# Kernel optimization log

Measured on AMD Instinct MI355X. Metric: run time of the kernel, lower is better.

Reference implementation:

```python
import jax, jax.numpy as jnp
import numpy as np

B, T, D_MODEL, HEAD_DIM = 4, 4096, 1024, 64

def setup_inputs() -> dict:
    key = jax.random.key(0)
    ks = jax.random.split(key, 7)
    s = 1.0 / np.sqrt(D_MODEL)
    return {
        "x": jax.random.normal(ks[0], (B, T, D_MODEL), dtype=jnp.float32),
        "Wq": jax.random.uniform(ks[1], (D_MODEL, HEAD_DIM), jnp.float32, -s, s),
        "bq": jax.random.uniform(ks[2], (HEAD_DIM,), jnp.float32, -s, s),
        "Wk": jax.random.uniform(ks[3], (D_MODEL, HEAD_DIM), jnp.float32, -s, s),
        "bk": jax.random.uniform(ks[4], (HEAD_DIM,), jnp.float32, -s, s),
        "Wv": jax.random.uniform(ks[5], (D_MODEL, HEAD_DIM), jnp.float32, -s, s),
        "bv": jax.random.uniform(ks[6], (HEAD_DIM,), jnp.float32, -s, s),
    }

def reference(x, Wq, bq, Wk, bk, Wv, bv):
    # x: [B,T,D]; projections -> [B,T,H]
    q = jnp.einsum("btd,dh->bth", x, Wq) + bq
    k = jnp.einsum("btd,dh->bth", x, Wk) + bk
    v = jnp.einsum("btd,dh->bth", x, Wv) + bv
    scale = HEAD_DIM ** -0.5
    # scores: [B,Tq,Tk] -- naive full attention matrix (memory-bound)
    scores = jnp.einsum("bqh,bkh->bqk", q, k) * scale
    neg = jnp.finfo(scores.dtype).min
    T_ = scores.shape[-1]
    causal = jnp.triu(jnp.full((T_, T_), neg, dtype=scores.dtype), k=1)
    scores = scores + causal[None, :, :]
    probs = jax.nn.softmax(scores, axis=-1)
    y = jnp.einsum("bqk,bkh->bqh", probs, v)
    return y
```

## Files before the change

### kernel.cpp

```cpp
#include <hip/hip_runtime.h>
#include <hip/hip_bf16.h>

typedef __attribute__((ext_vector_type(4))) float f4v;
typedef __attribute__((ext_vector_type(16))) float f16v;
typedef __attribute__((ext_vector_type(4))) unsigned short u16x4;
typedef __attribute__((ext_vector_type(8))) unsigned short u16x8;
typedef __attribute__((ext_vector_type(4))) unsigned int u32x4;
typedef __attribute__((ext_vector_type(8))) __bf16 bf16x8;
typedef __attribute__((ext_vector_type(8))) _Float16 h8v;

#define D_MODEL 1024
#define HDIM 64
#define TSEQ 4096
#define QB 32
#define KVB 64
#define QSCALE 0.18033688011112042f

__device__ __forceinline__ unsigned short f2bf(float f) {
    union { float f; unsigned u; } v; v.f = f;
    unsigned r = v.u + 0x7FFFu + ((v.u >> 16) & 1u);
    return (unsigned short)(r >> 16);
}
__device__ __forceinline__ bf16x8 ld8(const unsigned short* p) {
    return __builtin_bit_cast(bf16x8, *(const u16x8*)p);
}
__device__ __forceinline__ h8v ldh8(const unsigned short* p) {
    return __builtin_bit_cast(h8v, *(const u16x8*)p);
}
__device__ __forceinline__ f4v mfma16f(h8v a, h8v b, f4v c) {
    return __builtin_amdgcn_mfma_f32_16x16x32_f16(a, b, c, 0, 0, 0);
}
__device__ __forceinline__ f16v mfma32(bf16x8 a, bf16x8 b, f16v c) {
    return __builtin_amdgcn_mfma_f32_32x32x16_bf16(a, b, c, 0, 0, 0);
}
__device__ __forceinline__ unsigned cvtpk(float a, float b) {
    unsigned r;
    asm("v_cvt_pk_bf16_f32 %0, %1, %2" : "=v"(r) : "v"(a), "v"(b));
    return r;
}
__device__ __forceinline__ void pswap(unsigned& a, unsigned& b) {
    asm("v_permlane32_swap_b32 %0, %1" : "+v"(a), "+v"(b));
}
__device__ __forceinline__ h8v pack8(f4v a, f4v b) {
    unsigned p0 = __builtin_bit_cast(unsigned, __builtin_amdgcn_cvt_pkrtz(a[0], a[1]));
    unsigned p1 = __builtin_bit_cast(unsigned, __builtin_amdgcn_cvt_pkrtz(a[2], a[3]));
    unsigned p2 = __builtin_bit_cast(unsigned, __builtin_amdgcn_cvt_pkrtz(b[0], b[1]));
    unsigned p3 = __builtin_bit_cast(unsigned, __builtin_amdgcn_cvt_pkrtz(b[2], b[3]));
    u32x4 u = {p0, p1, p2, p3};
    return __builtin_bit_cast(h8v, u);
}

__global__ void prep_wf(const float* __restrict__ Wq, const float* __restrict__ Wk,
                        const float* __restrict__ Wv, unsigned short* __restrict__ Wf)
{
    int idx = blockIdx.x * 256 + threadIdx.x;
    int j = idx & 7, lane = (idx >> 3) & 63, nf = (idx >> 9) & 3,
        kstep = (idx >> 11) & 31, m = idx >> 16;
    int k = kstep * 32 + 8 * (lane >> 4) + j;
    int n = nf * 16 + (lane & 15);
    const float* W = (m == 0) ? Wq : (m == 1) ? Wk : Wv;
    _Float16 hv = (_Float16)W[k * 64 + n];
    Wf[idx] = __builtin_bit_cast(unsigned short, hv);
}

__global__ __launch_bounds__(256, 2)
void proj_qkv(const float* __restrict__ x, const unsigned short* __restrict__ Wf,
              const float* __restrict__ bq, const float* __restrict__ bk,
              const float* __restrict__ bv,
              unsigned short* __restrict__ Qf, unsigned short* __restrict__ Kf,
              unsigned short* __restrict__ Vf)
{
    __shared__ float xs[2][2048];
    __shared__ unsigned short wl[2][12288];

    const int tid = threadIdx.x;
    const int w = tid >> 6, l = tid & 63;
    const int row0 = blockIdx.x * 32;

    f4v acc[2][3];
#pragma unroll
    for (int s = 0; s < 2; ++s)
#pragma unroll
        for (int f = 0; f < 3; ++f) acc[s][f] = (f4v)0.f;

    auto stage = [&](int buf, int t) {
#pragma unroll
        for (int j = 0; j < 2; ++j) {
            const int G = j * 256 + tid;
            const int row = G >> 4;
            const int gl = (G & 15) ^ (row & 7);
            const float* src = x + (size_t)(row0 + row) * D_MODEL + t * 64 + gl * 4;
            __builtin_amdgcn_global_load_lds(
                (const __attribute__((address_space(1))) unsigned*)src,
                (__attribute__((address_space(3))) unsigned*)&xs[buf][G * 4],
                16, 0, 0);
        }
#pragma unroll
        for (int j = 0; j < 6; ++j) {
            const int chunk = j * 4 + w;
            const int cf = chunk >> 1, ks = chunk & 1;
            const unsigned short* src =
                Wf + ((((cf >> 2) * 32 + (t * 2 + ks)) * 4 + (cf & 3)) << 9) + l * 8;
            __builtin_amdgcn_global_load_lds(
                (const __attribute__((address_space(1))) unsigned*)src,
                (__attribute__((address_space(3))) unsigned*)&wl[buf][chunk * 512],
                16, 0, 0);
        }
    };

    stage(0, 0);
    __syncthreads();

#pragma unroll
    for (int t = 0; t < 16; ++t) {
        if (t < 15) stage((t + 1) & 1, t + 1);
        const int b = t & 1;
        const int sw = l & 7;
#pragma unroll
        for (int ks = 0; ks < 2; ++ks) {
            h8v bw[3];
#pragma unroll
            for (int f = 0; f < 3; ++f) {
                const int cf = w * 3 + f;
                bw[f] = ldh8(&wl[b][(cf * 2 + ks) * 512 + l * 8]);
            }
            const int gr = ks * 8 + 2 * (l >> 4);
#pragma unroll
            for (int s = 0; s < 2; ++s) {
                const int row = s * 16 + (l & 15);
                f4v a0 = *(const f4v*)&xs[b][row * 64 + ((gr ^ sw) << 2)];
                f4v a1 = *(const f4v*)&xs[b][row * 64 + (((gr + 1) ^ sw) << 2)];
                h8v xa = pack8(a0, a1);
#pragma unroll
                for (int f = 0; f < 3; ++f)
                    acc[s][f] = mfma16f(xa, bw[f], acc[s][f]);
            }
        }
        __syncthreads();
    }

    const float* bias[3] = {bq, bk, bv};
#pragma unroll
    for (int s = 0; s < 2; ++s) {
        const int rowb = row0 + s * 16 + 4 * (l >> 4);
        const int b = rowb >> 12, tok0 = rowb & 4095;
#pragma unroll
        for (int f = 0; f < 3; ++f) {
            const int cf = w * 3 + f;
            const int m = cf >> 2, nf = cf & 3;
            const int d = nf * 16 + (l & 15);
            const float bb = bias[m][d];
            if (m == 0) {
                const int qtile = tok0 >> 5;
                const int ksq = d >> 4, hq = (d >> 3) & 1, jq = d & 7;
#pragma unroll
                for (int r4 = 0; r4 < 4; ++r4) {
                    int cq = (tok0 & 31) + r4;
                    Qf[(((size_t)(b * 128 + qtile) * 4 + ksq) << 9) + (32 * hq + cq) * 8 + jq] =
                        f2bf((acc[s][f][r4] + bb) * QSCALE);
                }
            } else if (m == 1) {
                const int t = tok0 >> 6, tb = (tok0 >> 5) & 1;
                const int ksk = d >> 4, hk = (d >> 3) & 1, jk = d & 7;
#pragma unroll
                for (int r4 = 0; r4 < 4; ++r4) {
                    int ck = (tok0 & 31) + r4;
                    Kf[(((size_t)((b * 64 + t) * 8 + tb * 4 + ksk)) << 9) + (32 * hk + ck) * 8 + jk] =
                        f2bf(acc[s][f][r4] + bb);
                }
            } else {
                const int t = tok0 >> 6, ku = (tok0 >> 4) & 3, hv = (tok0 >> 3) & 1, jv = tok0 & 7;
                const int cv = d & 31, td = d >> 5;
                u16x4 pk;
#pragma unroll
                for (int r4 = 0; r4 < 4; ++r4) pk[r4] = f2bf(acc[s][f][r4] + bb);
                *(u16x4*)(Vf + (((size_t)((b * 64 + t) * 8 + td * 4 + ku)) << 9) +
                          (32 * hv + cv) * 8 + jv) = pk;
            }
        }
    }
}

struct TState { float m, l; f16v o0, o1; };

__device__ __forceinline__ void run_tile(const unsigned short* __restrict__ Qf,
                                         const unsigned short* __restrict__ Kf,
                                         const unsigned short* __restrict__ Vf,
                                         int batch, int qt, int g8, int l, int h, int c,
                                         TState& st)
{
    const int NT = (qt >> 1) + 1;
    st.m = -1e30f; st.l = 0.f; st.o0 = (f16v)0.f; st.o1 = (f16v)0.f;

    bf16x8 qf[4];
    const unsigned short* qp = Qf + (((size_t)(batch * 128 + qt) * 4) << 9) + l * 8;
#pragma unroll
    for (int ks = 0; ks < 4; ++ks) qf[ks] = ld8(qp + (ks << 9));

    if (g8 >= NT) return;

    auto kload = [&](bf16x8(&kr)[2][4], int t_) {
        const unsigned short* p = Kf + (((size_t)(batch * 64 + t_) * 8) << 9) + l * 8;
#pragma unroll
        for (int tb = 0; tb < 2; ++tb)
#pragma unroll
            for (int ks = 0; ks < 4; ++ks)
                kr[tb][ks] = ld8(p + ((tb * 4 + ks) << 9));
    };

    auto body = [&](bf16x8(&kr)[2][4], bf16x8(&kn)[2][4], int t_) {
        bf16x8 vr[2][4];
        {
            const unsigned short* p = Vf + (((size_t)(batch * 64 + t_) * 8) << 9) + l * 8;
#pragma unroll
            for (int td = 0; td < 2; ++td)
#pragma unroll
                for (int ku = 0; ku < 4; ++ku)
                    vr[td][ku] = ld8(p + ((td * 4 + ku) << 9));
        }
        f16v sacc[2];
        sacc[0] = (f16v)0.f; sacc[1] = (f16v)0.f;
#pragma unroll
        for (int ks = 0; ks < 4; ++ks) {
            sacc[0] = mfma32(kr[0][ks], qf[ks], sacc[0]);
            sacc[1] = mfma32(kr[1][ks], qf[ks], sacc[1]);
        }
        int tn = t_ + 8; if (tn > NT - 1) tn = NT - 1;
        kload(kn, tn);
        if (t_ == NT - 1) {
            const int off = qt * QB - t_ * KVB;
#pragma unroll
            for (int tb = 0; tb < 2; ++tb)
#pragma unroll
                for (int r = 0; r < 16; ++r) {
                    int mv = 32 * tb + (r & 3) + 8 * (r >> 2) + 4 * h - off;
                    if (mv > c) sacc[tb][r] = -1e30f;
                }
        }
        float pm = -1e30f;
#pragma unroll
        for (int tb = 0; tb < 2; ++tb)
#pragma unroll
            for (int r = 0; r < 16; ++r) pm = fmaxf(pm, sacc[tb][r]);
        pm = fmaxf(pm, __shfl_xor(pm, 32));
        const float mnew = fmaxf(st.m, pm);
        const float sc = exp2f(st.m - mnew);
        st.m = mnew;
        float rs = 0.f;
        float p[2][16];
#pragma unroll
        for (int tb = 0; tb < 2; ++tb)
#pragma unroll
            for (int r = 0; r < 16; ++r) {
                float e = exp2f(sacc[tb][r] - mnew);
                p[tb][r] = e; rs += e;
            }
        rs += __shfl_xor(rs, 32);
        st.l = st.l * sc + rs;
#pragma unroll
        for (int r = 0; r < 16; ++r) { st.o0[r] *= sc; st.o1[r] *= sc; }
        bf16x8 pa[4];
#pragma unroll
        for (int tb = 0; tb < 2; ++tb) {
            unsigned wp[8];
#pragma unroll
            for (int i = 0; i < 8; ++i) wp[i] = cvtpk(p[tb][2 * i], p[tb][2 * i + 1]);
            pswap(wp[0], wp[2]); pswap(wp[1], wp[3]);
            pswap(wp[4], wp[6]); pswap(wp[5], wp[7]);
            u32x4 f0 = {wp[0], wp[1], wp[2], wp[3]};
            u32x4 f1 = {wp[4], wp[5], wp[6], wp[7]};
            pa[2 * tb]     = __builtin_bit_cast(bf16x8, f0);
            pa[2 * tb + 1] = __builtin_bit_cast(bf16x8, f1);
        }
#pragma unroll
        for (int ku = 0; ku < 4; ++ku) {
            st.o0 = mfma32(vr[0][ku], pa[ku], st.o0);
            st.o1 = mfma32(vr[1][ku], pa[ku], st.o1);
        }
    };

    bf16x8 kA[2][4], kB[2][4];
    int t = g8;
    kload(kA, t);
    for (;;) {
        body(kA, kB, t);
        t += 8; if (t >= NT) break;
        body(kB, kA, t);
        t += 8; if (t >= NT) break;
    }
}

__global__ __launch_bounds__(512, 2)
void attn(const unsigned short* __restrict__ Qf, const unsigned short* __restrict__ Kf,
          const unsigned short* __restrict__ Vf, float* __restrict__ Yg)
{
    __shared__ float Osm[8][QB][33];
    __shared__ float Msm[2][8][QB];
    __shared__ float Lsm[2][8][QB];

    const int tid = threadIdx.x;
    const int g8 = tid >> 6, l = tid & 63, h = l >> 5, c = l & 31;
    const int batch = blockIdx.x & 3;
    const int pr = blockIdx.x >> 2;
    const int qtA = pr, qtB = 127 - pr;

    TState sB, sA;
    run_tile(Qf, Kf, Vf, batch, qtB, g8, l, h, c, sB);
    run_tile(Qf, Kf, Vf, batch, qtA, g8, l, h, c, sA);

    if (h == 0) {
        Msm[0][g8][c] = sA.m; Lsm[0][g8][c] = sA.l;
        Msm[1][g8][c] = sB.m; Lsm[1][g8][c] = sB.l;
    }

    auto write_partial = [&](const f16v& o) {
#pragma unroll
        for (int r = 0; r < 16; ++r) {
            int dd = (r & 3) + 8 * (r >> 2) + 4 * h;
            Osm[g8][c][dd] = o[r];
        }
    };
    auto merge_phase = [&](int tile, int dhalf, int qt_) {
        const int q = tid >> 4, d2 = (tid & 15) * 2;
        float mm = -1e30f;
#pragma unroll
        for (int gg = 0; gg < 8; ++gg) mm = fmaxf(mm, Msm[tile][gg][q]);
        float L = 0.f, o0 = 0.f, o1 = 0.f;
#pragma unroll
        for (int gg = 0; gg < 8; ++gg) {
            float a = exp2f(Msm[tile][gg][q] - mm);
            L += a * Lsm[tile][gg][q];
            o0 += a * Osm[gg][q][d2];
            o1 += a * Osm[gg][q][d2 + 1];
        }
        float inv = 1.f / L;
        float* yp = Yg + ((size_t)batch * TSEQ + (size_t)qt_ * QB + q) * HDIM + dhalf * 32 + d2;
        yp[0] = o0 * inv; yp[1] = o1 * inv;
    };

    write_partial(sA.o0);
    __syncthreads();
    merge_phase(0, 0, qtA);
    __syncthreads();
    write_partial(sA.o1);
    __syncthreads();
    merge_phase(0, 1, qtA);
    __syncthreads();
    write_partial(sB.o0);
    __syncthreads();
    merge_phase(1, 0, qtB);
    __syncthreads();
    write_partial(sB.o1);
    __syncthreads();
    merge_phase(1, 1, qtB);
}

extern "C" void kernel_launch(void* const* d_in, const int* in_sizes, int n_in,
                              void* d_out, int out_size, void* d_ws, size_t ws_size,
                              hipStream_t stream)
{
    const float* x  = (const float*)d_in[0];
    const float* Wq = (const float*)d_in[1];
    const float* bq = (const float*)d_in[2];
    const float* Wk = (const float*)d_in[3];
    const float* bk = (const float*)d_in[4];
    const float* Wv = (const float*)d_in[5];
    const float* bv = (const float*)d_in[6];
    float* y = (float*)d_out;

    unsigned short* Qb = (unsigned short*)d_ws;
    unsigned short* Kb = Qb + (size_t)1048576;
    unsigned short* Vb = Kb + (size_t)1048576;
    unsigned short* Wf = Vb + (size_t)1048576;

    prep_wf<<<768, 256, 0, stream>>>(Wq, Wk, Wv, Wf);
    proj_qkv<<<512, 256, 0, stream>>>(x, Wf, bq, bk, bv, Qb, Kb, Vb);
    attn<<<256, 512, 0, stream>>>(Qb, Kb, Vb, y);
}
```

Baseline: 50.43 us.

## Launch one causal tile per block, largest first, with MFMA priority hints

Each attention block used to process a paired short and long causal query tile back to back. Now each block handles a single tile, launched in descending work order (qt = 127 - blockIdx/4), with twice as many blocks. Launch bounds are raised to four blocks per CU, and s_setprio brackets the MFMA loops. The aim is finer-grained load balancing and more occupancy, relying on the hardware scheduler to drain work in order, at the cost of tighter register limits that could cause spills.

```diff
diff --git a/kernel.cpp b/kernel.cpp
--- a/kernel.cpp
+++ b/kernel.cpp
@@ -220,11 +220,13 @@
         }
         f16v sacc[2];
         sacc[0] = (f16v)0.f; sacc[1] = (f16v)0.f;
+        __builtin_amdgcn_s_setprio(1);
 #pragma unroll
         for (int ks = 0; ks < 4; ++ks) {
             sacc[0] = mfma32(kr[0][ks], qf[ks], sacc[0]);
             sacc[1] = mfma32(kr[1][ks], qf[ks], sacc[1]);
         }
+        __builtin_amdgcn_s_setprio(0);
         int tn = t_ + 8; if (tn > NT - 1) tn = NT - 1;
         kload(kn, tn);
         if (t_ == NT - 1) {
@@ -272,11 +274,13 @@
             pa[2 * tb]     = __builtin_bit_cast(bf16x8, f0);
             pa[2 * tb + 1] = __builtin_bit_cast(bf16x8, f1);
         }
+        __builtin_amdgcn_s_setprio(1);
 #pragma unroll
         for (int ku = 0; ku < 4; ++ku) {
             st.o0 = mfma32(vr[0][ku], pa[ku], st.o0);
             st.o1 = mfma32(vr[1][ku], pa[ku], st.o1);
         }
+        __builtin_amdgcn_s_setprio(0);
     };
 
     bf16x8 kA[2][4], kB[2][4];
@@ -290,28 +294,23 @@
     }
 }
 
-__global__ __launch_bounds__(512, 2)
+__global__ __launch_bounds__(512, 4)
 void attn(const unsigned short* __restrict__ Qf, const unsigned short* __restrict__ Kf,
           const unsigned short* __restrict__ Vf, float* __restrict__ Yg)
 {
     __shared__ float Osm[8][QB][33];
-    __shared__ float Msm[2][8][QB];
-    __shared__ float Lsm[2][8][QB];
+    __shared__ float Msm[8][QB];
+    __shared__ float Lsm[8][QB];
 
     const int tid = threadIdx.x;
     const int g8 = tid >> 6, l = tid & 63, h = l >> 5, c = l & 31;
     const int batch = blockIdx.x & 3;
-    const int pr = blockIdx.x >> 2;
-    const int qtA = pr, qtB = 127 - pr;
-
-    TState sB, sA;
-    run_tile(Qf, Kf, Vf, batch, qtB, g8, l, h, c, sB);
-    run_tile(Qf, Kf, Vf, batch, qtA, g8, l, h, c, sA);
-
-    if (h == 0) {
-        Msm[0][g8][c] = sA.m; Lsm[0][g8][c] = sA.l;
-        Msm[1][g8][c] = sB.m; Lsm[1][g8][c] = sB.l;
-    }
+    const int qt = 127 - (blockIdx.x >> 2);
+
+    TState st;
+    run_tile(Qf, Kf, Vf, batch, qt, g8, l, h, c, st);
+
+    if (h == 0) { Msm[g8][c] = st.m; Lsm[g8][c] = st.l; }
 
     auto write_partial = [&](const f16v& o) {
 #pragma unroll
@@ -320,39 +319,31 @@
             Osm[g8][c][dd] = o[r];
         }
     };
-    auto merge_phase = [&](int tile, int dhalf, int qt_) {
+    auto merge_phase = [&](int dhalf) {
         const int q = tid >> 4, d2 = (tid & 15) * 2;
         float mm = -1e30f;
 #pragma unroll
-        for (int gg = 0; gg < 8; ++gg) mm = fmaxf(mm, Msm[tile][gg][q]);
+        for (int gg = 0; gg < 8; ++gg) mm = fmaxf(mm, Msm[gg][q]);
         float L = 0.f, o0 = 0.f, o1 = 0.f;
 #pragma unroll
         for (int gg = 0; gg < 8; ++gg) {
-            float a = exp2f(Msm[tile][gg][q] - mm);
-            L += a * Lsm[tile][gg][q];
+            float a = exp2f(Msm[gg][q] - mm);
+            L += a * Lsm[gg][q];
             o0 += a * Osm[gg][q][d2];
             o1 += a * Osm[gg][q][d2 + 1];
         }
         float inv = 1.f / L;
-        float* yp = Yg + ((size_t)batch * TSEQ + (size_t)qt_ * QB + q) * HDIM + dhalf * 32 + d2;
+        float* yp = Yg + ((size_t)batch * TSEQ + (size_t)qt * QB + q) * HDIM + dhalf * 32 + d2;
         yp[0] = o0 * inv; yp[1] = o1 * inv;
     };
 
-    write_partial(sA.o0);
+    write_partial(st.o0);
     __syncthreads();
-    merge_phase(0, 0, qtA);
+    merge_phase(0);
     __syncthreads();
-    write_partial(sA.o1);
+    write_partial(st.o1);
     __syncthreads();
-    merge_phase(0, 1, qtA);
-    __syncthreads();
-    write_partial(sB.o0);
-    __syncthreads();
-    merge_phase(1, 0, qtB);
-    __syncthreads();
-    write_partial(sB.o1);
-    __syncthreads();
-    merge_phase(1, 1, qtB);
+    merge_phase(1);
 }
 
 extern "C" void kernel_launch(void* const* d_in, const int* in_sizes, int n_in,
@@ -375,5 +366,5 @@
 
     prep_wf<<<768, 256, 0, stream>>>(Wq, Wk, Wv, Wf);
     proj_qkv<<<512, 256, 0, stream>>>(x, Wf, bq, bk, bv, Qb, Kb, Vb);
-    attn<<<256, 512, 0, stream>>>(Qb, Kb, Vb, y);
-}
+    attn<<<512, 512, 0, stream>>>(Qb, Kb, Vb, y);
+}
```

Measured after the change: 142.2 us. 2.82x slower.
